# Optimization experiments

Measured on AMD Instinct MI355X. Metric: run time of the kernel, lower is better.

Reference implementation:

```python
import jax, jax.numpy as jnp
import numpy as np

N_NODES = 100000
N_EDGES = 1600000
N_ETYPES = 3
IN_FEATS = 128
HEADS = 4
OUT_FEATS = 16
EDGE_FEATS = 64
NEG_SLOPE = 0.2


def setup_inputs() -> dict:
    key = jax.random.key(0)
    ks = jax.random.split(key, 10)
    return {
        "x": jax.random.normal(ks[0], (N_NODES, IN_FEATS), jnp.float32),
        "W": jax.random.normal(ks[1], (IN_FEATS, HEADS * OUT_FEATS), jnp.float32) * 0.05,
        "W_e": jax.random.normal(ks[2], (EDGE_FEATS, HEADS * EDGE_FEATS), jnp.float32) * 0.05,
        "attn_l": jax.random.normal(ks[3], (HEADS, OUT_FEATS), jnp.float32) * 0.1,
        "attn_r": jax.random.normal(ks[4], (HEADS, OUT_FEATS), jnp.float32) * 0.1,
        "attn_e": jax.random.normal(ks[5], (HEADS, EDGE_FEATS), jnp.float32) * 0.1,
        "edge_emb": jax.random.normal(ks[6], (N_ETYPES, EDGE_FEATS), jnp.float32),
        "src": jax.random.randint(ks[7], (N_EDGES,), 0, N_NODES, jnp.int32),
        "dst": jax.random.randint(ks[8], (N_EDGES,), 0, N_NODES, jnp.int32),
        "etype": jax.random.randint(ks[9], (N_EDGES,), 0, N_ETYPES, jnp.int32),
    }


def reference(x, W, W_e, attn_l, attn_r, attn_e, edge_emb, src, dst, etype):
    N = x.shape[0]
    H, D = attn_l.shape
    # node projection: [N, H, D]
    feat = (x @ W).reshape(N, H, D)
    # per-node attention halves: [N, H]
    el = jnp.einsum("nhd,hd->nh", feat, attn_l)
    er = jnp.einsum("nhd,hd->nh", feat, attn_r)
    # per-etype edge term: [T, H]
    e_feat = (edge_emb @ W_e).reshape(edge_emb.shape[0], H, -1)
    ee = jnp.einsum("the,he->th", e_feat, attn_e)
    # per-edge pre-softmax score: [E, H]
    s = el[src] + er[dst] + ee[etype]
    s = jnp.where(s > 0, s, NEG_SLOPE * s)  # leaky_relu
    # edge softmax over incoming edges of each dst node (homogeneous graph)
    m = jax.ops.segment_max(s, dst, num_segments=N)
    e = jnp.exp(s - m[dst])
    z = jax.ops.segment_sum(e, dst, num_segments=N)
    a = e / z[dst]  # [E, H]
    # u_mul_e + sum aggregation: [N, H, D]
    msg = feat[src] * a[:, :, None]
    rst = jax.ops.segment_sum(msg, dst, num_segments=N)
    return rst, a
```

## Files before the change

### kernel.cpp

```cpp
#include <hip/hip_runtime.h>
#include <hip/hip_bf16.h>

#define N_NODES   100000
#define N_EDGES   1600000
#define N_ETYPES  3
#define IN_FEATS  128
#define HEADS     4
#define OUT_FEATS 16
#define EDGE_FEATS 64
#define HD        64
#define NEG_SLOPE 0.2f
#define MAXD_LDS  128

#define NBUCK     800
#define NPB       125
#define PBLK      400
#define EPB       4000
#define BCAP      2560


typedef short s16x8 __attribute__((ext_vector_type(8)));
typedef float f32x4 __attribute__((ext_vector_type(4)));

__device__ __forceinline__ short f2bs(float f) {
    __hip_bfloat16 h = __float2bfloat16(f);
    return *reinterpret_cast<short*>(&h);
}

#define XS_STRIDE 136
__global__ __launch_bounds__(256) void feat_el_er_kernel(
    const float* __restrict__ x,
    const float* __restrict__ W,
    const float* __restrict__ attn_l,
    const float* __restrict__ attn_r,
    const float* __restrict__ edge_emb,
    const float* __restrict__ W_e,
    const float* __restrict__ attn_e,
    __hip_bfloat16* __restrict__ featb,
    float* __restrict__ el,
    float* __restrict__ eriz,
    float* __restrict__ ee,
    int* __restrict__ cnt)
{
    const int t = threadIdx.x;

    if (blockIdx.x == N_NODES / 16) {
        for (int j = t; j < NBUCK; j += 256) cnt[j] = 0;
        const int wv = t >> 6, e = t & 63;
        for (int j = wv; j < N_ETYPES * HEADS; j += 4) {
            const int ty = j >> 2, h = j & 3;
            float ef = 0.f;
#pragma unroll
            for (int k = 0; k < EDGE_FEATS; ++k)
                ef += edge_emb[ty * EDGE_FEATS + k] *
                      W_e[k * (HEADS * EDGE_FEATS) + h * EDGE_FEATS + e];
            float v = ef * attn_e[h * EDGE_FEATS + e];
#pragma unroll
            for (int m = 1; m < 64; m <<= 1) v += __shfl_xor(v, m, 64);
            if (e == 0) ee[ty * HEADS + h] = v;
        }
        return;
    }

    __shared__ short Xs[16 * XS_STRIDE];
    __shared__ short Ws[64 * XS_STRIDE];

    const int row0 = blockIdx.x * 16;
    {
        const int r = t >> 4, k0 = (t & 15) * 8;
        const float4* xg = (const float4*)(x + (size_t)(row0 + r) * IN_FEATS + k0);
        const float4 v0 = xg[0], v1 = xg[1];
        s16x8 p;
        p[0] = f2bs(v0.x); p[1] = f2bs(v0.y); p[2] = f2bs(v0.z); p[3] = f2bs(v0.w);
        p[4] = f2bs(v1.x); p[5] = f2bs(v1.y); p[6] = f2bs(v1.z); p[7] = f2bs(v1.w);
        *(s16x8*)&Xs[r * XS_STRIDE + k0] = p;
    }
    {
        const int n  = t & 63;
        const int kb = (t >> 6) * 32;
#pragma unroll
        for (int kk = 0; kk < 32; kk += 8) {
            s16x8 p;
#pragma unroll
            for (int j = 0; j < 8; ++j)
                p[j] = f2bs(W[(size_t)(kb + kk + j) * HD + n]);
            *(s16x8*)&Ws[n * XS_STRIDE + kb + kk] = p;
        }
    }
    __syncthreads();

    const int w    = t >> 6;
    const int lane = t & 63;
    const int m    = lane & 15;
    const int q    = lane >> 4;

    f32x4 acc = {0.f, 0.f, 0.f, 0.f};
#pragma unroll
    for (int kb = 0; kb < 4; ++kb) {
        const s16x8 af = *(const s16x8*)&Xs[m * XS_STRIDE + kb * 32 + q * 8];
        const s16x8 bf = *(const s16x8*)&Ws[(w * 16 + m) * XS_STRIDE + kb * 32 + q * 8];
        acc = __builtin_amdgcn_mfma_f32_16x16x32_bf16(af, bf, acc, 0, 0, 0);
    }

    const float al = attn_l[w * OUT_FEATS + m];
    const float ar = attn_r[w * OUT_FEATS + m];
#pragma unroll
    for (int r = 0; r < 4; ++r) {
        const int row = row0 + q * 4 + r;
        featb[(size_t)row * HD + w * 16 + m] = __float2bfloat16(acc[r]);
        float cl = acc[r] * al;
        float cr = acc[r] * ar;
#pragma unroll
        for (int msk = 1; msk < 16; msk <<= 1) {
            cl += __shfl_xor(cl, msk, 64);
            cr += __shfl_xor(cr, msk, 64);
        }
        if (m == 0) {
            el[row * HEADS + w] = cl;
            eriz[(size_t)row * 8 + w] = cr;
        }
    }
}

__global__ __launch_bounds__(256) void scatter_kernel(
    const int* __restrict__ src, const int* __restrict__ dst,
    const int* __restrict__ etype,
    int* __restrict__ cnt, int* __restrict__ sc_bucket)
{
    __shared__ int h[NBUCK];
    const int t = threadIdx.x, b = blockIdx.x;
    for (int j = t; j < NBUCK; j += 256) h[j] = 0;
    __syncthreads();
    const int e0 = b * EPB;
    for (int i = t; i < EPB; i += 256)
        atomicAdd(&h[dst[e0 + i] / NPB], 1);
    __syncthreads();
    for (int j = t; j < NBUCK; j += 256) {
        const int c = h[j];
        h[j] = j * BCAP + (c ? atomicAdd(&cnt[j], c) : 0);
    }
    __syncthreads();
    for (int i = t; i < EPB; i += 256) {
        const int e  = e0 + i;
        const int dn = dst[e];
        const int bu = dn / NPB;
        const int ld = dn - bu * NPB;
        const int slot = atomicAdd(&h[bu], 1);
        sc_bucket[slot] = src[e] | (etype[e] << 17) | (ld << 19);
    }
}

__global__ __launch_bounds__(256) void bucket_csr_kernel(
    const int* __restrict__ sc_bucket, const int* __restrict__ cnt,
    int* __restrict__ ptr, int* __restrict__ sc_csr)
{
    __shared__ int sbuf[BCAP];
    __shared__ int sdeg[128];
    __shared__ int scur[128];
    __shared__ int red[4];
    const int t = threadIdx.x, b = blockIdx.x;

    int acc = 0;
    for (int j = t; j < b; j += 256) acc += cnt[j];
#pragma unroll
    for (int m = 1; m < 64; m <<= 1) acc += __shfl_xor(acc, m, 64);
    if ((t & 63) == 0) red[t >> 6] = acc;
    if (t < 128) sdeg[t] = 0;
    __syncthreads();
    const int lo    = red[0] + red[1] + red[2] + red[3];
    const int count = cnt[b];
    const int base  = b * BCAP;
    const bool staged = (count <= BCAP);

    if (staged) {
        for (int i = t; i < count; i += 256) {
            const int v = sc_bucket[base + i];
            sbuf[i] = v;
            atomicAdd(&sdeg[(v >> 19) & 0x7F], 1);
        }
    } else {
        for (int i = t; i < count; i += 256)
            atomicAdd(&sdeg[(sc_bucket[base + i] >> 19) & 0x7F], 1);
    }
    __syncthreads();
    const int orig = (t < 128) ? sdeg[t] : 0;
    for (int off = 1; off < 128; off <<= 1) {
        const int v = (t < 128 && t >= off) ? sdeg[t - off] : 0;
        __syncthreads();
        if (t < 128) sdeg[t] += v;
        __syncthreads();
    }
    if (t < 128) {
        const int excl = sdeg[t] - orig;
        if (t < NPB) ptr[b * NPB + t] = lo + excl;
        scur[t] = lo + excl;
    }
    if (b == 0 && t == 0) ptr[N_NODES] = N_EDGES;
    __syncthreads();
    if (staged) {
        for (int i = t; i < count; i += 256) {
            const int v = sbuf[i];
            const int ld = (v >> 19) & 0x7F;
            const int slot = atomicAdd(&scur[ld], 1);
            sc_csr[slot] = v & 0x7FFFF;
        }
    } else {
        for (int i = t; i < count; i += 256) {
            const int v = sc_bucket[base + i];
            const int ld = (v >> 19) & 0x7F;
            const int slot = atomicAdd(&scur[ld], 1);
            sc_csr[slot] = v & 0x7FFFF;
        }
    }
}

__global__ __launch_bounds__(256) void agg_kernel(
    const int* __restrict__ sc_csr, const int* __restrict__ ptr,
    const float* __restrict__ el, float* __restrict__ eriz,
    const float* __restrict__ ee, const __hip_bfloat16* __restrict__ featb,
    float* __restrict__ rst)
{
    __shared__ float w_lds[4][MAXD_LDS * HEADS];
    __shared__ int   s_lds[4][MAXD_LDS];
    const int wid  = threadIdx.x >> 6;
    const int lane = threadIdx.x & 63;
    const int n    = blockIdx.x * 4 + wid;

    const int p0  = ptr[n];
    const int deg = ptr[n + 1] - p0;
    float* wl = w_lds[wid];
    int*   sl = s_lds[wid];
    const ushort* fb = (const ushort*)featb;

    if (deg <= MAXD_LDS) {
        const int eo = lane >> 2;
        const int hA = lane & 3;
        const float er_n = eriz[(size_t)n * 8 + hA];
        const float g0 = ee[hA], g1 = ee[HEADS + hA], g2 = ee[2 * HEADS + hA];

        float zacc = 0.f;
        for (int i0 = 0; i0 < deg; i0 += 16) {
            const int idx = i0 + eo;
            if (idx < deg) {
                const int v  = sc_csr[p0 + idx];
                const int sn = v & 0x1FFFF;
                const int ty = v >> 17;
                float s = el[sn * HEADS + hA] + er_n +
                          ((ty == 0) ? g0 : ((ty == 1) ? g1 : g2));
                s = s > 0.f ? s : NEG_SLOPE * s;
                const float w = __expf(s);
                wl[idx * HEADS + hA] = w;
                if (hA == 0) sl[idx] = sn;
                zacc += w;
            }
        }
        zacc += __shfl_xor(zacc, 4, 64);
        zacc += __shfl_xor(zacc, 8, 64);
        zacc += __shfl_xor(zacc, 16, 64);
        zacc += __shfl_xor(zacc, 32, 64);
        if (lane < 4)
            eriz[(size_t)n * 8 + 4 + lane] = (deg > 0) ? __frcp_rn(zacc) : 0.f;

        const int q8 = lane >> 3;
        const int c8 = lane & 7;
        const int h8 = c8 >> 1;
        const float inv_z = (deg > 0) ? __frcp_rn(__shfl(zacc, h8, 64)) : 0.f;

        float a0 = 0.f, a1 = 0.f, a2 = 0.f, a3 = 0.f;
        float a4 = 0.f, a5 = 0.f, a6 = 0.f, a7 = 0.f;
        int i = 0;
        for (; i + 8 <= deg; i += 8) {
            const int idx = i + q8;
            const int sA = sl[idx];
            const float wA = wl[idx * HEADS + h8];
            const uint4 fA = *(const uint4*)(fb + ((size_t)sA << 6) + (c8 << 3));
            a0 += __uint_as_float(fA.x << 16) * wA;
            a1 += __uint_as_float(fA.x & 0xFFFF0000u) * wA;
            a2 += __uint_as_float(fA.y << 16) * wA;
            a3 += __uint_as_float(fA.y & 0xFFFF0000u) * wA;
            a4 += __uint_as_float(fA.z << 16) * wA;
            a5 += __uint_as_float(fA.z & 0xFFFF0000u) * wA;
            a6 += __uint_as_float(fA.w << 16) * wA;
            a7 += __uint_as_float(fA.w & 0xFFFF0000u) * wA;
        }
        if (i + q8 < deg) {
            const int idx = i + q8;
            const int sA = sl[idx];
            const float wA = wl[idx * HEADS + h8];
            const uint4 fA = *(const uint4*)(fb + ((size_t)sA << 6) + (c8 << 3));
            a0 += __uint_as_float(fA.x << 16) * wA;
            a1 += __uint_as_float(fA.x & 0xFFFF0000u) * wA;
            a2 += __uint_as_float(fA.y << 16) * wA;
            a3 += __uint_as_float(fA.y & 0xFFFF0000u) * wA;
            a4 += __uint_as_float(fA.z << 16) * wA;
            a5 += __uint_as_float(fA.z & 0xFFFF0000u) * wA;
            a6 += __uint_as_float(fA.w << 16) * wA;
            a7 += __uint_as_float(fA.w & 0xFFFF0000u) * wA;
        }
        a0 += __shfl_xor(a0, 8, 64); a0 += __shfl_xor(a0, 16, 64); a0 += __shfl_xor(a0, 32, 64);
        a1 += __shfl_xor(a1, 8, 64); a1 += __shfl_xor(a1, 16, 64); a1 += __shfl_xor(a1, 32, 64);
        a2 += __shfl_xor(a2, 8, 64); a2 += __shfl_xor(a2, 16, 64); a2 += __shfl_xor(a2, 32, 64);
        a3 += __shfl_xor(a3, 8, 64); a3 += __shfl_xor(a3, 16, 64); a3 += __shfl_xor(a3, 32, 64);
        a4 += __shfl_xor(a4, 8, 64); a4 += __shfl_xor(a4, 16, 64); a4 += __shfl_xor(a4, 32, 64);
        a5 += __shfl_xor(a5, 8, 64); a5 += __shfl_xor(a5, 16, 64); a5 += __shfl_xor(a5, 32, 64);
        a6 += __shfl_xor(a6, 8, 64); a6 += __shfl_xor(a6, 16, 64); a6 += __shfl_xor(a6, 32, 64);
        a7 += __shfl_xor(a7, 8, 64); a7 += __shfl_xor(a7, 16, 64); a7 += __shfl_xor(a7, 32, 64);
        if (q8 == 0) {
            f32x4 v0 = {a0 * inv_z, a1 * inv_z, a2 * inv_z, a3 * inv_z};
            f32x4 v1 = {a4 * inv_z, a5 * inv_z, a6 * inv_z, a7 * inv_z};
            *(f32x4*)(rst + (size_t)n * HD + (c8 << 3))     = v0;
            *(f32x4*)(rst + (size_t)n * HD + (c8 << 3) + 4) = v1;
        }
    } else {
        const int hA = lane & 3;
        const int eo = lane >> 2;
        const float er_nA = eriz[(size_t)n * 8 + hA];
        const float a0 = ee[hA], a1 = ee[HEADS + hA], a2 = ee[2 * HEADS + hA];
        float zacc = 0.f;
        for (int base = 0; base < deg; base += 16) {
            const int idx = base + eo;
            if (idx < deg) {
                const int v  = sc_csr[p0 + idx];
                const int sn = v & 0x1FFFF;
                const int ty = v >> 17;
                float s = el[sn * HEADS + hA] + er_nA + ((ty == 0) ? a0 : ((ty == 1) ? a1 : a2));
                s = s > 0.f ? s : NEG_SLOPE * s;
                zacc += __expf(s);
            }
        }
#pragma unroll
        for (int m = 4; m < 64; m <<= 1) zacc += __shfl_xor(zacc, m, 64);
        if (lane < 4) eriz[(size_t)n * 8 + 4 + lane] = __frcp_rn(zacc);
        const int h = lane >> 4;
        const float inv_z = __frcp_rn(__shfl(zacc, h, 64));
        const float er_n = eriz[(size_t)n * 8 + h];
        const float g0 = ee[h], g1 = ee[HEADS + h], g2 = ee[2 * HEADS + h];
        float racc = 0.f;
        for (int i = 0; i < deg; ++i) {
            const int v  = sc_csr[p0 + i];
            const int sn = v & 0x1FFFF;
            const int ty = v >> 17;
            float s = el[sn * HEADS + h] + er_n + ((ty == 0) ? g0 : ((ty == 1) ? g1 : g2));
            s = s > 0.f ? s : NEG_SLOPE * s;
            const float a = __expf(s) * inv_z;
            racc += __bfloat162float(featb[(size_t)sn * HD + lane]) * a;
        }
        rst[(size_t)n * HD + lane] = racc;
    }
}

__global__ __launch_bounds__(256) void attn_out_kernel(
    const int* __restrict__ src, const int* __restrict__ dst,
    const int* __restrict__ etype,
    const float* __restrict__ el, const float* __restrict__ eriz,
    const float* __restrict__ ee,
    float* __restrict__ a_out)
{
    const int e = blockIdx.x * 256 + threadIdx.x;
    const int sN = src[e];
    const int dN = dst[e];
    const int ty = etype[e];
    const float4 l4 = *(const float4*)(el + (size_t)sN * HEADS);
    const float4 r4 = *(const float4*)(eriz + (size_t)dN * 8);
    const float4 iz = *(const float4*)(eriz + (size_t)dN * 8 + 4);
    const float4 g4 = *(const float4*)(ee + (size_t)ty * HEADS);
    float4 a;
    float s;
    s = l4.x + r4.x + g4.x; s = s > 0.f ? s : NEG_SLOPE * s; a.x = __expf(s) * iz.x;
    s = l4.y + r4.y + g4.y; s = s > 0.f ? s : NEG_SLOPE * s; a.y = __expf(s) * iz.y;
    s = l4.z + r4.z + g4.z; s = s > 0.f ? s : NEG_SLOPE * s; a.z = __expf(s) * iz.z;
    s = l4.w + r4.w + g4.w; s = s > 0.f ? s : NEG_SLOPE * s; a.w = __expf(s) * iz.w;
    *(float4*)(a_out + (size_t)e * HEADS) = a;
}

extern "C" void kernel_launch(void* const* d_in, const int* in_sizes, int n_in,
                              void* d_out, int out_size, void* d_ws, size_t ws_size,
                              hipStream_t stream)
{
    const float* x        = (const float*)d_in[0];
    const float* W        = (const float*)d_in[1];
    const float* W_e      = (const float*)d_in[2];
    const float* attn_l   = (const float*)d_in[3];
    const float* attn_r   = (const float*)d_in[4];
    const float* attn_e   = (const float*)d_in[5];
    const float* edge_emb = (const float*)d_in[6];
    const int* src   = (const int*)d_in[7];
    const int* dst   = (const int*)d_in[8];
    const int* etype = (const int*)d_in[9];

    float* out     = (float*)d_out;
    float* rst_out = out;
    float* a_out   = out + (size_t)N_NODES * HD;

    char* w = (char*)d_ws;
    __hip_bfloat16* featb = (__hip_bfloat16*)w; w += (size_t)N_NODES * HD * 2;
    float* el    = (float*)w;  w += (size_t)N_NODES * HEADS * 4;
    float* eriz  = (float*)w;  w += (size_t)N_NODES * 8 * 4;
    float* ee    = (float*)w;  w += 64;
    int*   ptr   = (int*)w;    w += (size_t)(N_NODES + 4) * 4;
    int*   cnt   = (int*)w;    w += (size_t)(NBUCK + 8) * 4;
    int*   sc_bucket = (int*)w; w += (size_t)NBUCK * BCAP * 4;
    int*   sc_csr    = (int*)w; w += (size_t)N_EDGES * 4;

    feat_el_er_kernel<<<N_NODES / 16 + 1, 256, 0, stream>>>(
        x, W, attn_l, attn_r, edge_emb, W_e, attn_e, featb, el, eriz, ee, cnt);

    scatter_kernel<<<PBLK, 256, 0, stream>>>(src, dst, etype, cnt, sc_bucket);

    bucket_csr_kernel<<<NBUCK, 256, 0, stream>>>(sc_bucket, cnt, ptr, sc_csr);

    agg_kernel<<<N_NODES / 4, 256, 0, stream>>>(
        sc_csr, ptr, el, eriz, ee, featb, rst_out);

    attn_out_kernel<<<N_EDGES / 256, 256, 0, stream>>>(
        src, dst, etype, el, eriz, ee, a_out);
}
```

Before: 279.3 us.

## Pretranspose W to bf16, double rows per block, cache buckets, privatize degree histograms

A small prep kernel converts W to a transposed bf16 buffer once. The projection kernel then loads its B fragments straight from that buffer into registers and processes 32 rows per block, which removes the per-block W conversion and its LDS staging. The scatter kernel keeps each edge's bucket and local-dst in registers so the second pass does not reload dst or redo the division. The CSR kernel uses per-wave LDS degree histograms to reduce atomic contention. The cost is one extra kernel launch and fewer projection blocks.

```diff
diff --git a/kernel.cpp b/kernel.cpp
--- a/kernel.cpp
+++ b/kernel.cpp
@@ -17,6 +17,7 @@
 #define PBLK      400
 #define EPB       4000
 #define BCAP      2560
+#define FROWS     32
 
 
 typedef short s16x8 __attribute__((ext_vector_type(8)));
@@ -27,10 +28,18 @@
     return *reinterpret_cast<short*>(&h);
 }
 
+__global__ __launch_bounds__(256) void wt_prep_kernel(
+    const float* __restrict__ W, short* __restrict__ WTb)
+{
+    const int t = blockIdx.x * 256 + threadIdx.x;
+    const int k = t >> 6, n = t & 63;
+    WTb[n * IN_FEATS + k] = f2bs(W[t]);
+}
+
 #define XS_STRIDE 136
 __global__ __launch_bounds__(256) void feat_el_er_kernel(
     const float* __restrict__ x,
-    const float* __restrict__ W,
+    const short* __restrict__ WTb,
     const float* __restrict__ attn_l,
     const float* __restrict__ attn_r,
     const float* __restrict__ edge_emb,
@@ -44,7 +53,7 @@
 {
     const int t = threadIdx.x;
 
-    if (blockIdx.x == N_NODES / 16) {
+    if (blockIdx.x == N_NODES / FROWS) {
         for (int j = t; j < NBUCK; j += 256) cnt[j] = 0;
         const int wv = t >> 6, e = t & 63;
         for (int j = wv; j < N_ETYPES * HEADS; j += 4) {
@@ -62,62 +71,60 @@
         return;
     }
 
-    __shared__ short Xs[16 * XS_STRIDE];
-    __shared__ short Ws[64 * XS_STRIDE];
-
-    const int row0 = blockIdx.x * 16;
+    __shared__ short Xs[FROWS * XS_STRIDE];
+
+    const int row0 = blockIdx.x * FROWS;
     {
-        const int r = t >> 4, k0 = (t & 15) * 8;
+        const int r = t >> 3, k0 = (t & 7) * 16;
         const float4* xg = (const float4*)(x + (size_t)(row0 + r) * IN_FEATS + k0);
-        const float4 v0 = xg[0], v1 = xg[1];
-        s16x8 p;
-        p[0] = f2bs(v0.x); p[1] = f2bs(v0.y); p[2] = f2bs(v0.z); p[3] = f2bs(v0.w);
-        p[4] = f2bs(v1.x); p[5] = f2bs(v1.y); p[6] = f2bs(v1.z); p[7] = f2bs(v1.w);
-        *(s16x8*)&Xs[r * XS_STRIDE + k0] = p;
-    }
-    {
-        const int n  = t & 63;
-        const int kb = (t >> 6) * 32;
-#pragma unroll
-        for (int kk = 0; kk < 32; kk += 8) {
-            s16x8 p;
-#pragma unroll
-            for (int j = 0; j < 8; ++j)
-                p[j] = f2bs(W[(size_t)(kb + kk + j) * HD + n]);
-            *(s16x8*)&Ws[n * XS_STRIDE + kb + kk] = p;
-        }
-    }
-    __syncthreads();
+        const float4 v0 = xg[0], v1 = xg[1], v2 = xg[2], v3 = xg[3];
+        s16x8 p0, p1;
+        p0[0] = f2bs(v0.x); p0[1] = f2bs(v0.y); p0[2] = f2bs(v0.z); p0[3] = f2bs(v0.w);
+        p0[4] = f2bs(v1.x); p0[5] = f2bs(v1.y); p0[6] = f2bs(v1.z); p0[7] = f2bs(v1.w);
+        p1[0] = f2bs(v2.x); p1[1] = f2bs(v2.y); p1[2] = f2bs(v2.z); p1[3] = f2bs(v2.w);
+        p1[4] = f2bs(v3.x); p1[5] = f2bs(v3.y); p1[6] = f2bs(v3.z); p1[7] = f2bs(v3.w);
+        *(s16x8*)&Xs[r * XS_STRIDE + k0]     = p0;
+        *(s16x8*)&Xs[r * XS_STRIDE + k0 + 8] = p1;
+    }
 
     const int w    = t >> 6;
     const int lane = t & 63;
     const int m    = lane & 15;
     const int q    = lane >> 4;
 
-    f32x4 acc = {0.f, 0.f, 0.f, 0.f};
-#pragma unroll
-    for (int kb = 0; kb < 4; ++kb) {
-        const s16x8 af = *(const s16x8*)&Xs[m * XS_STRIDE + kb * 32 + q * 8];
-        const s16x8 bf = *(const s16x8*)&Ws[(w * 16 + m) * XS_STRIDE + kb * 32 + q * 8];
-        acc = __builtin_amdgcn_mfma_f32_16x16x32_bf16(af, bf, acc, 0, 0, 0);
-    }
+    s16x8 bfr[4];
+#pragma unroll
+    for (int kb = 0; kb < 4; ++kb)
+        bfr[kb] = *(const s16x8*)(WTb + (size_t)(w * 16 + m) * IN_FEATS + kb * 32 + q * 8);
 
     const float al = attn_l[w * OUT_FEATS + m];
     const float ar = attn_r[w * OUT_FEATS + m];
-#pragma unroll
-    for (int r = 0; r < 4; ++r) {
-        const int row = row0 + q * 4 + r;
-        featb[(size_t)row * HD + w * 16 + m] = __float2bfloat16(acc[r]);
-        float cl = acc[r] * al;
-        float cr = acc[r] * ar;
-#pragma unroll
-        for (int msk = 1; msk < 16; msk <<= 1) {
-            cl += __shfl_xor(cl, msk, 64);
-            cr += __shfl_xor(cr, msk, 64);
-        }
-        if (m == 0) {
-            el[row * HEADS + w] = cl;
-            eriz[(size_t)row * 8 + w] = cr;
+
+    __syncthreads();
+
+#pragma unroll
+    for (int rg = 0; rg < 2; ++rg) {
+        f32x4 acc = {0.f, 0.f, 0.f, 0.f};
+#pragma unroll
+        for (int kb = 0; kb < 4; ++kb) {
+            const s16x8 af = *(const s16x8*)&Xs[(rg * 16 + m) * XS_STRIDE + kb * 32 + q * 8];
+            acc = __builtin_amdgcn_mfma_f32_16x16x32_bf16(af, bfr[kb], acc, 0, 0, 0);
+        }
+#pragma unroll
+        for (int r = 0; r < 4; ++r) {
+            const int row = row0 + rg * 16 + q * 4 + r;
+            featb[(size_t)row * HD + w * 16 + m] = __float2bfloat16(acc[r]);
+            float cl = acc[r] * al;
+            float cr = acc[r] * ar;
+#pragma unroll
+            for (int msk = 1; msk < 16; msk <<= 1) {
+                cl += __shfl_xor(cl, msk, 64);
+                cr += __shfl_xor(cr, msk, 64);
+            }
+            if (m == 0) {
+                el[row * HEADS + w] = cl;
+                eriz[(size_t)row * 8 + w] = cr;
+            }
         }
     }
 }
@@ -128,23 +135,30 @@
     int* __restrict__ cnt, int* __restrict__ sc_bucket)
 {
     __shared__ int h[NBUCK];
+    int buld[16];
     const int t = threadIdx.x, b = blockIdx.x;
     for (int j = t; j < NBUCK; j += 256) h[j] = 0;
     __syncthreads();
     const int e0 = b * EPB;
-    for (int i = t; i < EPB; i += 256)
-        atomicAdd(&h[dst[e0 + i] / NPB], 1);
+    int k = 0;
+    for (int i = t; i < EPB; i += 256, ++k) {
+        const int dn = dst[e0 + i];
+        const int bu = dn / NPB;
+        const int ld = dn - bu * NPB;
+        buld[k] = bu | (ld << 16);
+        atomicAdd(&h[bu], 1);
+    }
     __syncthreads();
     for (int j = t; j < NBUCK; j += 256) {
         const int c = h[j];
         h[j] = j * BCAP + (c ? atomicAdd(&cnt[j], c) : 0);
     }
     __syncthreads();
-    for (int i = t; i < EPB; i += 256) {
+    k = 0;
+    for (int i = t; i < EPB; i += 256, ++k) {
         const int e  = e0 + i;
-        const int dn = dst[e];
-        const int bu = dn / NPB;
-        const int ld = dn - bu * NPB;
+        const int bu = buld[k] & 0xFFFF;
+        const int ld = buld[k] >> 16;
         const int slot = atomicAdd(&h[bu], 1);
         sc_bucket[slot] = src[e] | (etype[e] << 17) | (ld << 19);
     }
@@ -155,17 +169,20 @@
     int* __restrict__ ptr, int* __restrict__ sc_csr)
 {
     __shared__ int sbuf[BCAP];
-    __shared__ int sdeg[128];
+    __shared__ int sdeg4[4][128];
+    __shared__ int sdg[128];
     __shared__ int scur[128];
     __shared__ int red[4];
     const int t = threadIdx.x, b = blockIdx.x;
+    const int wid = t >> 6;
 
     int acc = 0;
     for (int j = t; j < b; j += 256) acc += cnt[j];
 #pragma unroll
     for (int m = 1; m < 64; m <<= 1) acc += __shfl_xor(acc, m, 64);
-    if ((t & 63) == 0) red[t >> 6] = acc;
-    if (t < 128) sdeg[t] = 0;
+    if ((t & 63) == 0) red[wid] = acc;
+    sdeg4[0][t & 127] = 0; sdeg4[1][t & 127] = 0;
+    if (t < 128) { sdeg4[2][t] = 0; sdeg4[3][t] = 0; }
     __syncthreads();
     const int lo    = red[0] + red[1] + red[2] + red[3];
     const int count = cnt[b];
@@ -176,22 +193,27 @@
         for (int i = t; i < count; i += 256) {
             const int v = sc_bucket[base + i];
             sbuf[i] = v;
-            atomicAdd(&sdeg[(v >> 19) & 0x7F], 1);
+            atomicAdd(&sdeg4[wid][(v >> 19) & 0x7F], 1);
         }
     } else {
         for (int i = t; i < count; i += 256)
-            atomicAdd(&sdeg[(sc_bucket[base + i] >> 19) & 0x7F], 1);
-    }
-    __syncthreads();
-    const int orig = (t < 128) ? sdeg[t] : 0;
+            atomicAdd(&sdeg4[wid][(sc_bucket[base + i] >> 19) & 0x7F], 1);
+    }
+    __syncthreads();
+    int orig = 0;
+    if (t < 128) {
+        orig = sdeg4[0][t] + sdeg4[1][t] + sdeg4[2][t] + sdeg4[3][t];
+        sdg[t] = orig;
+    }
+    __syncthreads();
     for (int off = 1; off < 128; off <<= 1) {
-        const int v = (t < 128 && t >= off) ? sdeg[t - off] : 0;
+        const int v = (t < 128 && t >= off) ? sdg[t - off] : 0;
         __syncthreads();
-        if (t < 128) sdeg[t] += v;
+        if (t < 128) sdg[t] += v;
         __syncthreads();
     }
     if (t < 128) {
-        const int excl = sdeg[t] - orig;
+        const int excl = sdg[t] - orig;
         if (t < NPB) ptr[b * NPB + t] = lo + excl;
         scur[t] = lo + excl;
     }
@@ -399,11 +421,14 @@
     float* ee    = (float*)w;  w += 64;
     int*   ptr   = (int*)w;    w += (size_t)(N_NODES + 4) * 4;
     int*   cnt   = (int*)w;    w += (size_t)(NBUCK + 8) * 4;
+    short* WTb   = (short*)w;  w += (size_t)HD * IN_FEATS * 2;
     int*   sc_bucket = (int*)w; w += (size_t)NBUCK * BCAP * 4;
     int*   sc_csr    = (int*)w; w += (size_t)N_EDGES * 4;
 
-    feat_el_er_kernel<<<N_NODES / 16 + 1, 256, 0, stream>>>(
-        x, W, attn_l, attn_r, edge_emb, W_e, attn_e, featb, el, eriz, ee, cnt);
+    wt_prep_kernel<<<(IN_FEATS * HD) / 256, 256, 0, stream>>>(W, WTb);
+
+    feat_el_er_kernel<<<N_NODES / FROWS + 1, 256, 0, stream>>>(
+        x, WTb, attn_l, attn_r, edge_emb, W_e, attn_e, featb, el, eriz, ee, cnt);
 
     scatter_kernel<<<PBLK, 256, 0, stream>>>(src, dst, etype, cnt, sc_bucket);
 
```

Measured after the change: 278.7 us. No clear change (-0.2%).
